# Performance work log

Hardware: AMD Instinct MI355X
Metric: run time of the kernel (lower is better)

The kernel has to match this reference:

```python
import jax, jax.numpy as jnp
import numpy as np

MARGIN = 0.2
MEM = 1000  # memory_size
EPS = 1e-12  # F.normalize eps


def _nearest_ds(x, h, w):
    # torch F.interpolate(mode='nearest'): src_idx = floor(dst_idx * H / h)
    B, H, W = x.shape
    ri = (jnp.arange(h) * H) // h
    ci = (jnp.arange(w) * W) // w
    return x[:, ri][:, :, ci]


def _first_k(mask, k):
    # Deterministic stand-in for randperm sampling: keep the first k True entries.
    rank = jnp.cumsum(mask.astype(jnp.int32)) - 1
    return mask & (rank < k), rank


def setup_inputs() -> dict:
    key = jax.random.key(0)
    k = jax.random.split(key, 6)
    B, C, H, W = 8, 21, 512, 512
    D, h, w = 128, 128, 128
    return {
        "preds": jax.random.normal(k[0], (B, C, H, W), jnp.float32),
        "embeddings": jax.random.normal(k[1], (B, D, h, w), jnp.float32),
        "gts": jax.random.randint(k[2], (B, H, W), 0, 21, dtype=jnp.int32),
        "fsss_gts": jax.random.randint(k[3], (B, H, W), 0, 256, dtype=jnp.int32),
        "pos_memory": jax.random.normal(k[4], (MEM, D), jnp.float32),
        "neg_memory": jax.random.normal(k[5], (MEM, D), jnp.float32),
    }


def reference(preds, embeddings, gts, fsss_gts, pos_memory, neg_memory):
    B, D, h, w = embeddings.shape
    M = pos_memory.shape[0]

    # downsample label maps / predicted classes to the feature resolution (nearest)
    s_pred = _nearest_ds(jnp.argmax(preds, axis=1).astype(jnp.float32), h, w).reshape(-1)
    s_fsss = _nearest_ds(fsss_gts.astype(jnp.float32), h, w).reshape(-1)
    # s_gt is computed in the original but unused for the loss.

    # L2-normalize embeddings over channel dim, flatten to [N, D] (channel-last)
    norm = jnp.sqrt(jnp.sum(embeddings * embeddings, axis=1, keepdims=True))
    emb = embeddings / jnp.maximum(norm, EPS)
    E = emb.transpose(1, 0, 2, 3).reshape(D, -1).T  # [N, D], N = B*h*w

    pred_mask = s_pred != 0
    fsss_mask = (s_fsss != 0) & (s_fsss != 255)
    ignore_mask = s_fsss == 255
    anchor_mask = pred_mask & fsss_mask
    positive_mask = fsss_mask ^ anchor_mask
    negative_mask = pred_mask ^ ((fsss_mask | ignore_mask) & pred_mask)

    sel_anc, _ = _first_k(anchor_mask, M // 10)
    sel_pos, rank_pos = _first_k(positive_mask, M // 3)
    sel_neg, rank_neg = _first_k(negative_mask, M // 3)

    # circular-buffer update (ptr=0): scatter selected (detached) embeddings into slots rank%M
    Ed = jax.lax.stop_gradient(E)
    idx_pos = jnp.where(sel_pos, rank_pos % M, M)  # M -> dropped
    idx_neg = jnp.where(sel_neg, rank_neg % M, M)
    pos_mem = pos_memory.at[idx_pos].set(Ed, mode='drop')
    neg_mem = neg_memory.at[idx_neg].set(Ed, mode='drop')

    # mean over all (anchor, memory) similarity pairs factorizes:
    # mean_{a,m} a.m = (sum_a a) . (sum_m m) / (Na * M)
    anc_sum = jnp.einsum('nd,n->d', E, sel_anc.astype(E.dtype))
    n_anc = jnp.maximum(jnp.sum(sel_anc.astype(E.dtype)), 1.0)
    pos_mean = jnp.dot(anc_sum, jnp.sum(pos_mem, axis=0)) / (n_anc * M)
    neg_mean = jnp.dot(anc_sum, jnp.sum(neg_mem, axis=0)) / (n_anc * M)

    return jax.nn.relu(pos_mean - neg_mean + MARGIN)
```

## Files before the change

### kernel.cpp

```cpp
#include <hip/hip_runtime.h>
#include <stdint.h>


#define NPOS  131072
#define NBLK  512
#define MEMSZ 1000
#define KANC  100
#define KPN   333
#define SLOT_POS 100
#define SLOT_NEG 433
#define NSLOTS 766
#define FIX_SCALE 1099511627776.0
#define INV_FIX   (1.0 / 1099511627776.0)

__global__ __launch_bounds__(256) void mask_kernel(
    const float* __restrict__ preds,
    const int* __restrict__ fsss,
    uint8_t* __restrict__ flags,
    int* __restrict__ blockCounts)
{
    const int tid = threadIdx.x, blk = blockIdx.x;
    const int lane = tid & 63, wave = tid >> 6;
    const int n = blk * 256 + tid;
    const int b = n >> 14;
    const int ij = n & 16383;
    const int row = (ij >> 7) << 2;
    const int col = (ij & 127) << 2;

    const float* p = preds + (size_t)b * 21 * 262144 + (size_t)row * 512 + col;
    float best = p[0];
    int bc = 0;
#pragma unroll
    for (int c = 1; c < 21; ++c) {
        float v = p[(size_t)c * 262144];
        if (v > best) { best = v; bc = c; }
    }
    const int fv = fsss[(size_t)b * 262144 + (size_t)row * 512 + col];

    const bool pm = (bc != 0);
    const bool fm = (fv != 0) && (fv != 255);
    const int myflag = (int)(pm && fm)
                     | ((int)(!pm && fm) << 1)
                     | ((int)(pm && (fv == 0)) << 2);
    flags[n] = (uint8_t)myflag;

    __shared__ int s_i[12];
#pragma unroll
    for (int cat = 0; cat < 3; ++cat) {
        unsigned long long m = __ballot((myflag >> cat) & 1);
        if (lane == 0) s_i[cat * 4 + wave] = (int)__popcll(m);
    }
    __syncthreads();
    if (tid < 3)
        blockCounts[tid * NBLK + blk] =
            s_i[tid * 4] + s_i[tid * 4 + 1] + s_i[tid * 4 + 2] + s_i[tid * 4 + 3];
}

__global__ __launch_bounds__(256) void select_kernel(
    const uint8_t* __restrict__ flags,
    const int* __restrict__ blockCounts,
    int* __restrict__ idx,
    int* __restrict__ totals,
    unsigned long long* __restrict__ accum)
{
    const int tid = threadIdx.x, blk = blockIdx.x;
    const int lane = tid & 63, wave = tid >> 6;
    __shared__ int s_i[12];

#pragma unroll
    for (int cat = 0; cat < 3; ++cat) {
        const int c0 = blockCounts[cat * NBLK + tid];
        const int c1 = blockCounts[cat * NBLK + 256 + tid];
        int v = ((tid < blk) ? c0 : 0) + ((256 + tid < blk) ? c1 : 0);
#pragma unroll
        for (int off = 1; off < 64; off <<= 1) v += __shfl_xor(v, off, 64);
        if (lane == 0) s_i[cat * 4 + wave] = v;
    }
    __syncthreads();
    int pre[3];
#pragma unroll
    for (int cat = 0; cat < 3; ++cat)
        pre[cat] = s_i[cat * 4] + s_i[cat * 4 + 1] + s_i[cat * 4 + 2] + s_i[cat * 4 + 3];
    if (blk == NBLK - 1 && tid < 3)
        totals[tid] = pre[tid] + blockCounts[tid * NBLK + NBLK - 1];

    if (blk == 0)
        for (int i = tid; i < 4 * 3 * 128; i += 256) accum[i] = 0ull;

    __syncthreads();

    const int n = blk * 256 + tid;
    const int f = flags[n];
    unsigned long long masks[3];
#pragma unroll
    for (int cat = 0; cat < 3; ++cat) {
        masks[cat] = __ballot((f >> cat) & 1);
        if (lane == 0) s_i[cat * 4 + wave] = (int)__popcll(masks[cat]);
    }
    __syncthreads();
    const int kcap[3] = {KANC, KPN, KPN};
    const int basec[3] = {0, SLOT_POS, SLOT_NEG};
#pragma unroll
    for (int cat = 0; cat < 3; ++cat) {
        if ((f >> cat) & 1) {
            int woff = 0;
#pragma unroll
            for (int w = 0; w < 4; ++w) if (w < wave) woff += s_i[cat * 4 + w];
            const int intra = woff + (int)__popcll(masks[cat] & ((1ull << lane) - 1ull));
            const int rank = pre[cat] + intra;
            if (rank < kcap[cat]) idx[basec[cat] + rank] = n;
        }
    }
}

__global__ __launch_bounds__(256) void gather_kernel(
    const float* __restrict__ emb,
    const float* __restrict__ posMem,
    const float* __restrict__ negMem,
    const int* __restrict__ idx,
    const int* __restrict__ totals,
    unsigned long long* __restrict__ accum)
{
    const int tid = threadIdx.x, blk = blockIdx.x;
    const int lane = tid & 63, wave = tid >> 6;
    const int d = tid & 127;
    const int A = min(KANC, totals[0]);
    const int P = min(KPN, totals[1]);
    const int Q = min(KPN, totals[2]);

    if (blk < 383) {
        const int half = tid >> 7;
        const int slot = blk * 2 + half;
        int cat; bool valid;
        if (slot < SLOT_POS)      { cat = 0; valid = slot < A; }
        else if (slot < SLOT_NEG) { cat = 1; valid = (slot - SLOT_POS) < P; }
        else                      { cat = 2; valid = (slot - SLOT_NEG) < Q; }

        float v = 0.f;
        if (valid) {
            const int nn = idx[slot];
            v = emb[((size_t)(nn >> 14) * 128 + d) * 16384 + (nn & 16383)];
        }
        float sq = v * v;
#pragma unroll
        for (int off = 1; off < 64; off <<= 1) sq += __shfl_xor(sq, off, 64);
        __shared__ float s_f[4];
        if (lane == 0) s_f[wave] = sq;
        __syncthreads();
        const float nrm2 = s_f[half * 2] + s_f[half * 2 + 1];
        if (valid) {
            const float scale = 1.0f / fmaxf(sqrtf(nrm2), 1e-12f);
            const double val = (double)v * (double)scale;
            const long long fx = (long long)llrint(val * FIX_SCALE);
            atomicAdd(&accum[(((size_t)(blk & 3) * 3 + cat) << 7) + d],
                      (unsigned long long)fx);
        }
    } else {
        const int t = blk - 383;
        const int memSel = t >> 3;
        const int part = t & 7;
        const float* mem = memSel ? negMem : posMem;
        const int cnt = memSel ? Q : P;
        const int rowHalf = tid >> 7;
        const int m0 = part * 125;
        double acc = 0.0;
        for (int r = rowHalf; r < 125; r += 2) {
            const int m = m0 + r;
            if (m >= cnt) acc += (double)mem[(size_t)m * 128 + d];
        }
        const long long fx = (long long)llrint(acc * FIX_SCALE);
        atomicAdd(&accum[(((size_t)(blk & 3) * 3 + (memSel ? 2 : 1)) << 7) + d],
                  (unsigned long long)fx);
    }
}

__global__ __launch_bounds__(128) void final_kernel(
    const unsigned long long* __restrict__ accum,
    const int* __restrict__ totals,
    float* __restrict__ out)
{
    const int d = threadIdx.x;
    const int lane = d & 63, wave = d >> 6;
    double anc = 0.0, pos = 0.0, neg = 0.0;
#pragma unroll
    for (int s = 0; s < 4; ++s) {
        anc += (double)(long long)accum[((s * 3 + 0) << 7) + d];
        pos += (double)(long long)accum[((s * 3 + 1) << 7) + d];
        neg += (double)(long long)accum[((s * 3 + 2) << 7) + d];
    }
    double prod = anc * (pos - neg) * (INV_FIX * INV_FIX);
#pragma unroll
    for (int off = 1; off < 64; off <<= 1) prod += __shfl_xor(prod, off, 64);
    __shared__ double s_d[2];
    if (lane == 0) s_d[wave] = prod;
    __syncthreads();
    if (d == 0) {
        const double red = s_d[0] + s_d[1];
        const int A = min(KANC, totals[0]);
        const double nAnc = (A > 0) ? (double)A : 1.0;
        const double vv = red / (nAnc * (double)MEMSZ) + 0.2;
        out[0] = (float)(vv > 0.0 ? vv : 0.0);
    }
}

extern "C" void kernel_launch(void* const* d_in, const int* in_sizes, int n_in,
                              void* d_out, int out_size, void* d_ws, size_t ws_size,
                              hipStream_t stream) {
    const float* preds  = (const float*)d_in[0];
    const float* emb    = (const float*)d_in[1];
    const int* fsss     = (const int*)d_in[3];
    const float* posMem = (const float*)d_in[4];
    const float* negMem = (const float*)d_in[5];
    float* out = (float*)d_out;

    char* ws = (char*)d_ws;
    uint8_t* flags   = (uint8_t*)ws;
    int* blockCounts = (int*)(ws + 131072);
    int* idx         = blockCounts + 3 * NBLK;
    int* totals      = idx + 768;
    unsigned long long* accum =
        (unsigned long long*)(ws + 131072 + (3 * NBLK + 768 + 4) * 4 + 4);
    accum = (unsigned long long*)(((uintptr_t)accum + 7) & ~(uintptr_t)7);

    mask_kernel  <<<NBLK, 256, 0, stream>>>(preds, fsss, flags, blockCounts);
    select_kernel<<<NBLK, 256, 0, stream>>>(flags, blockCounts, idx, totals, accum);
    gather_kernel<<<399, 256, 0, stream>>>(emb, posMem, negMem, idx, totals, accum);
    final_kernel <<<1, 128, 0, stream>>>(accum, totals, out);
}
```

Measured before the change: 41.04 us.

## Fuse four kernels into two using last-block-done atomic counters

Folds the selection pass into the mask kernel: the last block to finish, detected with an atomic counter, does the block-count scan and a serial flag scan that writes the first-k indices. It also folds the final reduction into the gather kernel with a second last-block counter, and adds a memset to zero the accumulators and counters. This removes two launches and the full second pass over flags, but the selection now runs serially in a single block and adds fences and a memset launch.

Result: slower. 158.5 us (+286.1%).

```diff
diff --git a/kernel.cpp b/kernel.cpp
--- a/kernel.cpp
+++ b/kernel.cpp
@@ -9,15 +9,26 @@
 #define KPN   333
 #define SLOT_POS 100
 #define SLOT_NEG 433
-#define NSLOTS 766
 #define FIX_SCALE 1099511627776.0
 #define INV_FIX   (1.0 / 1099511627776.0)
 
-__global__ __launch_bounds__(256) void mask_kernel(
+#define OFF_FLAGS   0
+#define OFF_COUNTS  131072
+#define OFF_IDX     137216
+#define OFF_TOTALS  140288
+#define OFF_ACCUM   140304
+#define OFF_CTRS    152592
+#define ZERO_BASE   OFF_ACCUM
+#define ZERO_BYTES  (12288 + 8)
+
+__global__ __launch_bounds__(256) void mask_select_kernel(
     const float* __restrict__ preds,
     const int* __restrict__ fsss,
     uint8_t* __restrict__ flags,
-    int* __restrict__ blockCounts)
+    int* __restrict__ blockCounts,
+    int* __restrict__ idx,
+    int* __restrict__ totals,
+    unsigned int* __restrict__ counterA)
 {
     const int tid = threadIdx.x, blk = blockIdx.x;
     const int lane = tid & 63, wave = tid >> 6;
@@ -54,72 +65,78 @@
     if (tid < 3)
         blockCounts[tid * NBLK + blk] =
             s_i[tid * 4] + s_i[tid * 4 + 1] + s_i[tid * 4 + 2] + s_i[tid * 4 + 3];
+
+    __threadfence();
+    __syncthreads();
+    __shared__ int s_fin;
+    if (tid == 0) {
+        unsigned old = atomicAdd(counterA, 1u);
+        s_fin = (old == NBLK - 1) ? 1 : 0;
+    }
+    __syncthreads();
+    if (!s_fin) return;
+    __threadfence();
+
+    __shared__ int s_pre[3 * NBLK];
+    __shared__ int s_w[4];
+#pragma unroll 1
+    for (int cat = 0; cat < 3; ++cat) {
+        const int c0 = blockCounts[cat * NBLK + 2 * tid];
+        const int c1 = blockCounts[cat * NBLK + 2 * tid + 1];
+        const int pairsum = c0 + c1;
+        int incl = pairsum;
+#pragma unroll
+        for (int off = 1; off < 64; off <<= 1) {
+            int v = __shfl_up(incl, off, 64);
+            if (lane >= off) incl += v;
+        }
+        if (lane == 63) s_w[wave] = incl;
+        __syncthreads();
+        int woff = 0;
+#pragma unroll
+        for (int w = 0; w < 4; ++w) if (w < wave) woff += s_w[w];
+        const int excl0 = woff + incl - pairsum;
+        s_pre[cat * NBLK + 2 * tid]     = excl0;
+        s_pre[cat * NBLK + 2 * tid + 1] = excl0 + c0;
+        if (tid == 0) totals[cat] = s_w[0] + s_w[1] + s_w[2] + s_w[3];
+        __syncthreads();
+    }
+
+    const int kcap[3]  = {KANC, KPN, KPN};
+    const int basec[3] = {0, SLOT_POS, SLOT_NEG};
+#pragma unroll 1
+    for (int cat = 0; cat < 3; ++cat) {
+        const int cap = kcap[cat];
+#pragma unroll 1
+        for (int h = 0; h < 2; ++h) {
+            const int bb = 2 * tid + h;
+            int rank = s_pre[cat * NBLK + bb];
+            if (rank >= cap) continue;
+            const unsigned long long* f8 =
+                (const unsigned long long*)(flags + (size_t)bb * 256);
+#pragma unroll 1
+            for (int k8 = 0; k8 < 32 && rank < cap; ++k8) {
+                unsigned long long m = (f8[k8] >> cat) & 0x0101010101010101ull;
+                while (m) {
+                    const int bit = __ffsll((long long)m) - 1;
+                    idx[basec[cat] + rank] = bb * 256 + k8 * 8 + (bit >> 3);
+                    if (++rank >= cap) break;
+                    m &= m - 1;
+                }
+            }
+        }
+    }
 }
 
-__global__ __launch_bounds__(256) void select_kernel(
-    const uint8_t* __restrict__ flags,
-    const int* __restrict__ blockCounts,
-    int* __restrict__ idx,
-    int* __restrict__ totals,
-    unsigned long long* __restrict__ accum)
-{
-    const int tid = threadIdx.x, blk = blockIdx.x;
-    const int lane = tid & 63, wave = tid >> 6;
-    __shared__ int s_i[12];
-
-#pragma unroll
-    for (int cat = 0; cat < 3; ++cat) {
-        const int c0 = blockCounts[cat * NBLK + tid];
-        const int c1 = blockCounts[cat * NBLK + 256 + tid];
-        int v = ((tid < blk) ? c0 : 0) + ((256 + tid < blk) ? c1 : 0);
-#pragma unroll
-        for (int off = 1; off < 64; off <<= 1) v += __shfl_xor(v, off, 64);
-        if (lane == 0) s_i[cat * 4 + wave] = v;
-    }
-    __syncthreads();
-    int pre[3];
-#pragma unroll
-    for (int cat = 0; cat < 3; ++cat)
-        pre[cat] = s_i[cat * 4] + s_i[cat * 4 + 1] + s_i[cat * 4 + 2] + s_i[cat * 4 + 3];
-    if (blk == NBLK - 1 && tid < 3)
-        totals[tid] = pre[tid] + blockCounts[tid * NBLK + NBLK - 1];
-
-    if (blk == 0)
-        for (int i = tid; i < 4 * 3 * 128; i += 256) accum[i] = 0ull;
-
-    __syncthreads();
-
-    const int n = blk * 256 + tid;
-    const int f = flags[n];
-    unsigned long long masks[3];
-#pragma unroll
-    for (int cat = 0; cat < 3; ++cat) {
-        masks[cat] = __ballot((f >> cat) & 1);
-        if (lane == 0) s_i[cat * 4 + wave] = (int)__popcll(masks[cat]);
-    }
-    __syncthreads();
-    const int kcap[3] = {KANC, KPN, KPN};
-    const int basec[3] = {0, SLOT_POS, SLOT_NEG};
-#pragma unroll
-    for (int cat = 0; cat < 3; ++cat) {
-        if ((f >> cat) & 1) {
-            int woff = 0;
-#pragma unroll
-            for (int w = 0; w < 4; ++w) if (w < wave) woff += s_i[cat * 4 + w];
-            const int intra = woff + (int)__popcll(masks[cat] & ((1ull << lane) - 1ull));
-            const int rank = pre[cat] + intra;
-            if (rank < kcap[cat]) idx[basec[cat] + rank] = n;
-        }
-    }
-}
-
-__global__ __launch_bounds__(256) void gather_kernel(
+__global__ __launch_bounds__(256) void gather_final_kernel(
     const float* __restrict__ emb,
     const float* __restrict__ posMem,
     const float* __restrict__ negMem,
     const int* __restrict__ idx,
     const int* __restrict__ totals,
-    unsigned long long* __restrict__ accum)
+    unsigned long long* __restrict__ accum,
+    unsigned int* __restrict__ counterB,
+    float* __restrict__ out)
 {
     const int tid = threadIdx.x, blk = blockIdx.x;
     const int lane = tid & 63, wave = tid >> 6;
@@ -150,9 +167,9 @@
         const float nrm2 = s_f[half * 2] + s_f[half * 2 + 1];
         if (valid) {
             const float scale = 1.0f / fmaxf(sqrtf(nrm2), 1e-12f);
-            const double val = (double)v * (double)scale;
-            const long long fx = (long long)llrint(val * FIX_SCALE);
-            atomicAdd(&accum[(((size_t)(blk & 3) * 3 + cat) << 7) + d],
+            const long long fx =
+                (long long)llrint((double)v * (double)scale * FIX_SCALE);
+            atomicAdd(&accum[(((blk & 3) * 3 + cat) << 7) + d],
                       (unsigned long long)fx);
         }
     } else {
@@ -169,34 +186,38 @@
             if (m >= cnt) acc += (double)mem[(size_t)m * 128 + d];
         }
         const long long fx = (long long)llrint(acc * FIX_SCALE);
-        atomicAdd(&accum[(((size_t)(blk & 3) * 3 + (memSel ? 2 : 1)) << 7) + d],
+        atomicAdd(&accum[(((blk & 3) * 3 + (memSel ? 2 : 1)) << 7) + d],
                   (unsigned long long)fx);
     }
-}
-
-__global__ __launch_bounds__(128) void final_kernel(
-    const unsigned long long* __restrict__ accum,
-    const int* __restrict__ totals,
-    float* __restrict__ out)
-{
-    const int d = threadIdx.x;
-    const int lane = d & 63, wave = d >> 6;
-    double anc = 0.0, pos = 0.0, neg = 0.0;
-#pragma unroll
-    for (int s = 0; s < 4; ++s) {
-        anc += (double)(long long)accum[((s * 3 + 0) << 7) + d];
-        pos += (double)(long long)accum[((s * 3 + 1) << 7) + d];
-        neg += (double)(long long)accum[((s * 3 + 2) << 7) + d];
-    }
-    double prod = anc * (pos - neg) * (INV_FIX * INV_FIX);
-#pragma unroll
-    for (int off = 1; off < 64; off <<= 1) prod += __shfl_xor(prod, off, 64);
+
+    __threadfence();
+    __syncthreads();
+    __shared__ int s_fin;
+    if (tid == 0) {
+        unsigned old = atomicAdd(counterB, 1u);
+        s_fin = (old == 398) ? 1 : 0;
+    }
+    __syncthreads();
+    if (!s_fin) return;
+    __threadfence();
+
     __shared__ double s_d[2];
-    if (lane == 0) s_d[wave] = prod;
-    __syncthreads();
-    if (d == 0) {
+    if (tid < 128) {
+        double anc = 0.0, pos = 0.0, neg = 0.0;
+#pragma unroll
+        for (int s = 0; s < 4; ++s) {
+            anc += (double)(long long)accum[((s * 3 + 0) << 7) + tid];
+            pos += (double)(long long)accum[((s * 3 + 1) << 7) + tid];
+            neg += (double)(long long)accum[((s * 3 + 2) << 7) + tid];
+        }
+        double prod = anc * (pos - neg) * (INV_FIX * INV_FIX);
+#pragma unroll
+        for (int off = 1; off < 64; off <<= 1) prod += __shfl_xor(prod, off, 64);
+        if (lane == 0) s_d[wave] = prod;
+    }
+    __syncthreads();
+    if (tid == 0) {
         const double red = s_d[0] + s_d[1];
-        const int A = min(KANC, totals[0]);
         const double nAnc = (A > 0) ? (double)A : 1.0;
         const double vv = red / (nAnc * (double)MEMSZ) + 0.2;
         out[0] = (float)(vv > 0.0 ? vv : 0.0);
@@ -214,16 +235,17 @@
     float* out = (float*)d_out;
 
     char* ws = (char*)d_ws;
-    uint8_t* flags   = (uint8_t*)ws;
-    int* blockCounts = (int*)(ws + 131072);
-    int* idx         = blockCounts + 3 * NBLK;
-    int* totals      = idx + 768;
-    unsigned long long* accum =
-        (unsigned long long*)(ws + 131072 + (3 * NBLK + 768 + 4) * 4 + 4);
-    accum = (unsigned long long*)(((uintptr_t)accum + 7) & ~(uintptr_t)7);
-
-    mask_kernel  <<<NBLK, 256, 0, stream>>>(preds, fsss, flags, blockCounts);
-    select_kernel<<<NBLK, 256, 0, stream>>>(flags, blockCounts, idx, totals, accum);
-    gather_kernel<<<399, 256, 0, stream>>>(emb, posMem, negMem, idx, totals, accum);
-    final_kernel <<<1, 128, 0, stream>>>(accum, totals, out);
+    uint8_t* flags      = (uint8_t*)(ws + OFF_FLAGS);
+    int* blockCounts    = (int*)(ws + OFF_COUNTS);
+    int* idx            = (int*)(ws + OFF_IDX);
+    int* totals         = (int*)(ws + OFF_TOTALS);
+    unsigned long long* accum = (unsigned long long*)(ws + OFF_ACCUM);
+    unsigned int* ctrs  = (unsigned int*)(ws + OFF_CTRS);
+
+    hipMemsetAsync(ws + ZERO_BASE, 0, ZERO_BYTES, stream);
+
+    mask_select_kernel<<<NBLK, 256, 0, stream>>>(preds, fsss, flags, blockCounts,
+                                                 idx, totals, ctrs);
+    gather_final_kernel<<<399, 256, 0, stream>>>(emb, posMem, negMem, idx, totals,
+                                                 accum, ctrs + 1, out);
 }
```

## Fuse final reduction into gather via last-block counter; nontemporal mask loads

Applied to the files above, without the earlier changes.

Folds the single-block final reduction into the gather kernel: each block bumps a global atomic counter after a threadfence, and the last block to arrive reduces the accumulators and writes the output. This removes one kernel launch and its dependency gap. Zeroing of the accumulators and counter moves into mask_kernel. The strided preds and fsss loads in mask_kernel become nontemporal to avoid polluting the cache, at the cost of extra fence and atomic traffic in every gather block.

Result: slower. 50.37 us (+22.7%).

```diff
diff --git a/kernel.cpp b/kernel.cpp
--- a/kernel.cpp
+++ b/kernel.cpp
@@ -9,15 +9,23 @@
 #define KPN   333
 #define SLOT_POS 100
 #define SLOT_NEG 433
-#define NSLOTS 766
 #define FIX_SCALE 1099511627776.0
 #define INV_FIX   (1.0 / 1099511627776.0)
+
+#define OFF_FLAGS   0
+#define OFF_COUNTS  131072
+#define OFF_IDX     137216
+#define OFF_TOTALS  140288
+#define OFF_ACCUM   140304
+#define OFF_CTR     152592
 
 __global__ __launch_bounds__(256) void mask_kernel(
     const float* __restrict__ preds,
     const int* __restrict__ fsss,
     uint8_t* __restrict__ flags,
-    int* __restrict__ blockCounts)
+    int* __restrict__ blockCounts,
+    unsigned long long* __restrict__ accum,
+    unsigned int* __restrict__ counterB)
 {
     const int tid = threadIdx.x, blk = blockIdx.x;
     const int lane = tid & 63, wave = tid >> 6;
@@ -28,14 +36,15 @@
     const int col = (ij & 127) << 2;
 
     const float* p = preds + (size_t)b * 21 * 262144 + (size_t)row * 512 + col;
-    float best = p[0];
+    float best = __builtin_nontemporal_load(p);
     int bc = 0;
 #pragma unroll
     for (int c = 1; c < 21; ++c) {
-        float v = p[(size_t)c * 262144];
+        float v = __builtin_nontemporal_load(p + (size_t)c * 262144);
         if (v > best) { best = v; bc = c; }
     }
-    const int fv = fsss[(size_t)b * 262144 + (size_t)row * 512 + col];
+    const int fv = __builtin_nontemporal_load(
+        fsss + (size_t)b * 262144 + (size_t)row * 512 + col);
 
     const bool pm = (bc != 0);
     const bool fm = (fv != 0) && (fv != 255);
@@ -54,14 +63,18 @@
     if (tid < 3)
         blockCounts[tid * NBLK + blk] =
             s_i[tid * 4] + s_i[tid * 4 + 1] + s_i[tid * 4 + 2] + s_i[tid * 4 + 3];
+
+    if (blk == 0) {
+        for (int i = tid; i < 4 * 3 * 128; i += 256) accum[i] = 0ull;
+        if (tid == 0) *counterB = 0u;
+    }
 }
 
 __global__ __launch_bounds__(256) void select_kernel(
     const uint8_t* __restrict__ flags,
     const int* __restrict__ blockCounts,
     int* __restrict__ idx,
-    int* __restrict__ totals,
-    unsigned long long* __restrict__ accum)
+    int* __restrict__ totals)
 {
     const int tid = threadIdx.x, blk = blockIdx.x;
     const int lane = tid & 63, wave = tid >> 6;
@@ -83,10 +96,6 @@
         pre[cat] = s_i[cat * 4] + s_i[cat * 4 + 1] + s_i[cat * 4 + 2] + s_i[cat * 4 + 3];
     if (blk == NBLK - 1 && tid < 3)
         totals[tid] = pre[tid] + blockCounts[tid * NBLK + NBLK - 1];
-
-    if (blk == 0)
-        for (int i = tid; i < 4 * 3 * 128; i += 256) accum[i] = 0ull;
-
     __syncthreads();
 
     const int n = blk * 256 + tid;
@@ -98,7 +107,7 @@
         if (lane == 0) s_i[cat * 4 + wave] = (int)__popcll(masks[cat]);
     }
     __syncthreads();
-    const int kcap[3] = {KANC, KPN, KPN};
+    const int kcap[3]  = {KANC, KPN, KPN};
     const int basec[3] = {0, SLOT_POS, SLOT_NEG};
 #pragma unroll
     for (int cat = 0; cat < 3; ++cat) {
@@ -113,13 +122,15 @@
     }
 }
 
-__global__ __launch_bounds__(256) void gather_kernel(
+__global__ __launch_bounds__(256) void gather_final_kernel(
     const float* __restrict__ emb,
     const float* __restrict__ posMem,
     const float* __restrict__ negMem,
     const int* __restrict__ idx,
     const int* __restrict__ totals,
-    unsigned long long* __restrict__ accum)
+    unsigned long long* __restrict__ accum,
+    unsigned int* __restrict__ counterB,
+    float* __restrict__ out)
 {
     const int tid = threadIdx.x, blk = blockIdx.x;
     const int lane = tid & 63, wave = tid >> 6;
@@ -150,9 +161,9 @@
         const float nrm2 = s_f[half * 2] + s_f[half * 2 + 1];
         if (valid) {
             const float scale = 1.0f / fmaxf(sqrtf(nrm2), 1e-12f);
-            const double val = (double)v * (double)scale;
-            const long long fx = (long long)llrint(val * FIX_SCALE);
-            atomicAdd(&accum[(((size_t)(blk & 3) * 3 + cat) << 7) + d],
+            const long long fx =
+                (long long)llrint((double)v * (double)scale * FIX_SCALE);
+            atomicAdd(&accum[(((blk & 3) * 3 + cat) << 7) + d],
                       (unsigned long long)fx);
         }
     } else {
@@ -169,34 +180,38 @@
             if (m >= cnt) acc += (double)mem[(size_t)m * 128 + d];
         }
         const long long fx = (long long)llrint(acc * FIX_SCALE);
-        atomicAdd(&accum[(((size_t)(blk & 3) * 3 + (memSel ? 2 : 1)) << 7) + d],
+        atomicAdd(&accum[(((blk & 3) * 3 + (memSel ? 2 : 1)) << 7) + d],
                   (unsigned long long)fx);
     }
-}
-
-__global__ __launch_bounds__(128) void final_kernel(
-    const unsigned long long* __restrict__ accum,
-    const int* __restrict__ totals,
-    float* __restrict__ out)
-{
-    const int d = threadIdx.x;
-    const int lane = d & 63, wave = d >> 6;
-    double anc = 0.0, pos = 0.0, neg = 0.0;
-#pragma unroll
-    for (int s = 0; s < 4; ++s) {
-        anc += (double)(long long)accum[((s * 3 + 0) << 7) + d];
-        pos += (double)(long long)accum[((s * 3 + 1) << 7) + d];
-        neg += (double)(long long)accum[((s * 3 + 2) << 7) + d];
-    }
-    double prod = anc * (pos - neg) * (INV_FIX * INV_FIX);
-#pragma unroll
-    for (int off = 1; off < 64; off <<= 1) prod += __shfl_xor(prod, off, 64);
+
+    __threadfence();
+    __syncthreads();
+    __shared__ int s_fin;
+    if (tid == 0) {
+        unsigned old = atomicAdd(counterB, 1u);
+        s_fin = (old == 398) ? 1 : 0;
+    }
+    __syncthreads();
+    if (!s_fin) return;
+    __threadfence();
+
     __shared__ double s_d[2];
-    if (lane == 0) s_d[wave] = prod;
-    __syncthreads();
-    if (d == 0) {
+    if (tid < 128) {
+        double anc = 0.0, pos = 0.0, neg = 0.0;
+#pragma unroll
+        for (int s = 0; s < 4; ++s) {
+            anc += (double)(long long)accum[((s * 3 + 0) << 7) + tid];
+            pos += (double)(long long)accum[((s * 3 + 1) << 7) + tid];
+            neg += (double)(long long)accum[((s * 3 + 2) << 7) + tid];
+        }
+        double prod = anc * (pos - neg) * (INV_FIX * INV_FIX);
+#pragma unroll
+        for (int off = 1; off < 64; off <<= 1) prod += __shfl_xor(prod, off, 64);
+        if (lane == 0) s_d[wave] = prod;
+    }
+    __syncthreads();
+    if (tid == 0) {
         const double red = s_d[0] + s_d[1];
-        const int A = min(KANC, totals[0]);
         const double nAnc = (A > 0) ? (double)A : 1.0;
         const double vv = red / (nAnc * (double)MEMSZ) + 0.2;
         out[0] = (float)(vv > 0.0 ? vv : 0.0);
@@ -214,16 +229,16 @@
     float* out = (float*)d_out;
 
     char* ws = (char*)d_ws;
-    uint8_t* flags   = (uint8_t*)ws;
-    int* blockCounts = (int*)(ws + 131072);
-    int* idx         = blockCounts + 3 * NBLK;
-    int* totals      = idx + 768;
-    unsigned long long* accum =
-        (unsigned long long*)(ws + 131072 + (3 * NBLK + 768 + 4) * 4 + 4);
-    accum = (unsigned long long*)(((uintptr_t)accum + 7) & ~(uintptr_t)7);
-
-    mask_kernel  <<<NBLK, 256, 0, stream>>>(preds, fsss, flags, blockCounts);
-    select_kernel<<<NBLK, 256, 0, stream>>>(flags, blockCounts, idx, totals, accum);
-    gather_kernel<<<399, 256, 0, stream>>>(emb, posMem, negMem, idx, totals, accum);
-    final_kernel <<<1, 128, 0, stream>>>(accum, totals, out);
-}
+    uint8_t* flags      = (uint8_t*)(ws + OFF_FLAGS);
+    int* blockCounts    = (int*)(ws + OFF_COUNTS);
+    int* idx            = (int*)(ws + OFF_IDX);
+    int* totals         = (int*)(ws + OFF_TOTALS);
+    unsigned long long* accum = (unsigned long long*)(ws + OFF_ACCUM);
+    unsigned int* ctr   = (unsigned int*)(ws + OFF_CTR);
+
+    mask_kernel  <<<NBLK, 256, 0, stream>>>(preds, fsss, flags, blockCounts,
+                                            accum, ctr);
+    select_kernel<<<NBLK, 256, 0, stream>>>(flags, blockCounts, idx, totals);
+    gather_final_kernel<<<399, 256, 0, stream>>>(emb, posMem, negMem, idx, totals,
+                                                 accum, ctr, out);
+}
```
